# Kernel tuning notes

Measured on AMD Instinct MI355X. Metric: run time of the kernel, lower is better.

Reference implementation:

```python
import jax, jax.numpy as jnp
import numpy as np

B, T, D_MODEL, H, W = 2, 3, 32, 256, 256
N_HEADS, N_LEVELS, N_POINTS = 4, 3, 4


def conv2d(x, w, b, padding=1, dilation=1):
    y = jax.lax.conv_general_dilated(
        x, w, window_strides=(1, 1),
        padding=[(padding, padding), (padding, padding)],
        rhs_dilation=(dilation, dilation),
        dimension_numbers=('NCHW', 'OIHW', 'NCHW'))
    return y + b[None, :, None, None]


def lrelu(x):
    return jnp.where(x >= 0, x, 0.1 * x)


def bilinear_sample(img, x, y):
    # img: (N,C,H,W); x,y: (N,H',W') pixel coords; zero padding outside (grid_sample zeros)
    N, C, Hh, Ww = img.shape
    x0 = jnp.floor(x); y0 = jnp.floor(y)
    lx = x - x0; ly = y - y0
    imf = img.reshape(N, C, Hh * Ww)
    out = jnp.zeros((N, C) + x.shape[1:], img.dtype)
    for dy, dx, wgt in ((0, 0, (1 - lx) * (1 - ly)), (0, 1, lx * (1 - ly)),
                        (1, 0, (1 - lx) * ly), (1, 1, lx * ly)):
        xi = x0 + dx; yi = y0 + dy
        valid = (xi >= 0) & (xi < Ww) & (yi >= 0) & (yi < Hh)
        idx = (jnp.clip(yi, 0, Hh - 1) * Ww + jnp.clip(xi, 0, Ww - 1)).astype(jnp.int32)
        g = jnp.take_along_axis(imf, idx.reshape(N, 1, -1), axis=2).reshape((N, C) + x.shape[1:])
        out = out + g * (wgt * valid)[:, None]
    return out


def flow_warp(x, flow):
    # torch flow_warp with align_corners=True == sampling at pixel coords grid+flow
    N, C, Hh, Ww = x.shape
    gy, gx = jnp.meshgrid(jnp.arange(Hh, dtype=x.dtype), jnp.arange(Ww, dtype=x.dtype), indexing='ij')
    return bilinear_sample(x, gx[None] + flow[:, 0], gy[None] + flow[:, 1])


def ms_deform_attn(value, sampling_locations, attention_weights, h, w):
    # value: (N, L*h*w, Hh, d); loc: (N, Lq, Hh, L, P, 2) in [0,1]; weights: (N, Lq, Hh, L, P)
    # Matches MSDA CUDA kernel: sample at loc*(W,H)-0.5, bilinear, zero pad outside.
    N, _, Hh, d = value.shape
    Lq = sampling_locations.shape[1]
    L, P = sampling_locations.shape[3], sampling_locations.shape[4]
    out = jnp.zeros((N, Lq, Hh, d), value.dtype)
    for l in range(L):
        v = value[:, l * h * w:(l + 1) * h * w].transpose(0, 2, 1, 3)  # (N,Hh,hw,d)
        loc = sampling_locations[:, :, :, l]  # (N,Lq,Hh,P,2)
        x = loc[..., 0] * w - 0.5
        y = loc[..., 1] * h - 0.5
        x0 = jnp.floor(x); y0 = jnp.floor(y)
        lx = x - x0; ly = y - y0
        samp = jnp.zeros((N, Lq, Hh, P, d), value.dtype)
        for dy, dx, wgt in ((0, 0, (1 - lx) * (1 - ly)), (0, 1, lx * (1 - ly)),
                            (1, 0, (1 - lx) * ly), (1, 1, lx * ly)):
            xi = x0 + dx; yi = y0 + dy
            valid = (xi >= 0) & (xi < w) & (yi >= 0) & (yi < h)
            idx = (jnp.clip(yi, 0, h - 1) * w + jnp.clip(xi, 0, w - 1)).astype(jnp.int32)
            idx = idx.transpose(0, 2, 1, 3).reshape(N, Hh, Lq * P)
            g = jnp.take_along_axis(v, idx[..., None], axis=2)  # (N,Hh,Lq*P,d)
            g = g.reshape(N, Hh, Lq, P, d).transpose(0, 2, 1, 3, 4)
            samp = samp + g * (wgt * valid)[..., None]
        out = out + (samp * attention_weights[:, :, :, l][..., None]).sum(axis=3)
    return out.reshape(N, Lq, Hh * d)


def setup_inputs() -> dict:
    key = jax.random.key(0)
    ks = jax.random.split(key, 24)
    def rn(k, shape, s=1.0):
        return jax.random.normal(k, shape, dtype=jnp.float32) * s
    c = D_MODEL
    nofp = N_HEADS * N_LEVELS * N_POINTS
    return {
        'frame': rn(ks[0], (B, T, c, H, W)),
        'srcframe': rn(ks[1], (B, T, c, H, W)),
        'flow_forward': rn(ks[2], (B, T - 1, 2, H, W), 2.0),
        'flow_backward': rn(ks[3], (B, T - 1, 2, H, W), 2.0),
        'W_qk': rn(ks[4], (3 * c, 3 * c + 4, 3, 3), 0.05), 'b_qk': rn(ks[5], (3 * c,), 0.05),
        'W_v': rn(ks[6], (3 * c, 3 * c, 3, 3), 0.05), 'b_v': rn(ks[7], (3 * c,), 0.05),
        'W_vp': rn(ks[8], (c, c, 3, 3), 0.05), 'b_vp': rn(ks[9], (c,), 0.05),
        'W_off': rn(ks[10], (nofp * 2, 3 * c, 3, 3), 0.01), 'b_off': rn(ks[11], (nofp * 2,), 0.5),
        'W_aw': rn(ks[12], (nofp, 3 * c, 3, 3), 0.05), 'b_aw': rn(ks[13], (nofp,), 0.05),
        'W_out': rn(ks[14], (c, c, 3, 3), 0.05), 'b_out': rn(ks[15], (c,), 0.05),
        'W_ffd': rn(ks[16], (c, c, 3, 3), 0.05), 'b_ffd': rn(ks[17], (c,), 0.05),
        'W_ff1': rn(ks[18], (c, 2 * c, 3, 3), 0.05), 'b_ff1': rn(ks[19], (c,), 0.05),
        'W_ff2': rn(ks[20], (c, c, 3, 3), 0.05), 'b_ff2': rn(ks[21], (c,), 0.05),
        'W_fu': rn(ks[22], (c, c, 1, 1), 0.05), 'b_fu': rn(ks[23], (c,), 0.05),
    }


def reference(frame, srcframe, flow_forward, flow_backward,
              W_qk, b_qk, W_v, b_v, W_vp, b_vp, W_off, b_off, W_aw, b_aw,
              W_out, b_out, W_ffd, b_ffd, W_ff1, b_ff1, W_ff2, b_ff2, W_fu, b_fu):
    b, t, c, h, w = frame.shape
    Hh, L, P = N_HEADS, N_LEVELS, N_POINTS
    d = c // Hh
    # flow-warped neighbor frames + flows -> query embedding
    warp01 = flow_warp(frame[:, 0], flow_backward[:, 0])
    warp21 = flow_warp(frame[:, 2], flow_forward[:, 1])
    qk_in = jnp.concatenate([warp01, frame[:, 1], warp21,
                             flow_forward[:, 1], flow_backward[:, 0]], axis=1)
    qureys = lrelu(conv2d(qk_in, W_qk, b_qk))                       # (b, 3c, h, w)
    value = conv2d(frame.reshape(b, t * c, h, w), W_v, b_v)         # (b, 3c, h, w)
    # --- MSDeformAttn_Fusion ---
    val = conv2d(value.reshape(b * t, c, h, w), W_vp, b_vp).reshape(b, t, c, h, w)
    off = conv2d(qureys, W_off, b_off)                               # (b, Hh*L*P*2, h, w)
    aw = conv2d(qureys, W_aw, b_aw)                                  # (b, Hh*L*P, h, w)
    value_flat = val.reshape(b, t, c, h * w).transpose(0, 1, 3, 2).reshape(b, t * h * w, Hh, d)
    off = off.reshape(b, -1, h * w).transpose(0, 2, 1).reshape(b, h * w, Hh, L, P, 2)
    aw = aw.reshape(b, -1, h * w).transpose(0, 2, 1).reshape(b, h * w, Hh, L * P)
    aw = jax.nn.softmax(aw, axis=-1).reshape(b, h * w, Hh, L, P)
    # reference points: pixel centers normalized (masks all zero -> valid_ratios == 1)
    gy, gx = jnp.meshgrid((jnp.arange(h, dtype=off.dtype) + 0.5) / h,
                          (jnp.arange(w, dtype=off.dtype) + 0.5) / w, indexing='ij')
    ref = jnp.stack([gx.reshape(-1), gy.reshape(-1)], -1)            # (hw, 2) (x, y)
    normalizer = jnp.array([w, h], dtype=off.dtype)                  # same for all levels
    loc = ref[None, :, None, None, None, :] + off / normalizer
    attn_out = ms_deform_attn(value_flat, loc, aw, h, w)             # (b, hw, c)
    out = attn_out.reshape(b, h, w, c).transpose(0, 3, 1, 2)
    out = conv2d(out, W_out, b_out)                                  # output_proj
    # --- post-attention ---
    out = conv2d(out, W_ffd, b_ffd) + frame[:, 1]
    tseq = jnp.concatenate([out, srcframe[:, 1]], axis=1)            # (b, 2c, h, w)
    ff = conv2d(lrelu(conv2d(tseq, W_ff1, b_ff1, padding=2, dilation=2)), W_ff2, b_ff2)
    out = out + ff
    out = lrelu(conv2d(out, W_fu, b_fu, padding=0))                  # fusion 1x1
    return out
```

## Files before the change

kernel.cpp:

```cpp
#include <hip/hip_runtime.h>
#include <hip/hip_bf16.h>

typedef __hip_bfloat16 bf16;
typedef unsigned short us;
typedef unsigned int u32;
typedef __attribute__((ext_vector_type(8))) short short8;
typedef __attribute__((ext_vector_type(8))) unsigned short ushortx8;
typedef __attribute__((ext_vector_type(4))) float f32x4;
typedef __attribute__((ext_vector_type(16))) float f32x16;

#define HW 65536
#define IMW 256
#define IMH 256

static __device__ __forceinline__ float u2f(us u) {
  return __uint_as_float(((unsigned)u) << 16);
}
static __device__ __forceinline__ us f2bu(float x) {
  bf16 h = __float2bfloat16(x);
  return *reinterpret_cast<us*>(&h);
}
static __device__ __forceinline__ unsigned pk2(float a, float b) {
  return (unsigned)f2bu(a) | ((unsigned)f2bu(b) << 16);
}

static __device__ __forceinline__ void gload_lds16(const void* g, void* l) {
  __builtin_amdgcn_global_load_lds(
      (const __attribute__((address_space(1))) u32*)g,
      (__attribute__((address_space(3))) u32*)l, 16, 0, 0);
}

struct PrepArgs {
  const float* src[9];
  us* dst[9];
  int OC[9], CIN[9], KPAD[9], LAY[9];
};

__global__ __launch_bounds__(256) void prep_weights(PrepArgs a) {
  int j = blockIdx.y;
  int n = blockIdx.x * 256 + threadIdx.x;
  int OC = a.OC[j], CIN = a.CIN[j], KPAD = a.KPAD[j];
  int tot = 9 * OC * KPAD;
  if (n >= tot) return;
  int oc, k;
  if (a.LAY[j] == 0) {
    int G = OC >> 4, NKC = KPAD >> 5;
    int e = n & 7;
    int m = (n >> 3) & 15;
    int q = (n >> 7) & 3;
    int rest = n >> 9;
    int kc = rest % NKC;
    int tg = rest / NKC;
    int g = tg % G;
    int t = tg / G;
    oc = g * 16 + m;
    k = kc * 32 + q * 8 + e;
    float v = (k < CIN) ? a.src[j][(size_t)(oc * CIN + k) * 9 + t] : 0.f;
    a.dst[j][n] = f2bu(v);
  } else {
    int OCT = OC >> 5, KH = KPAD >> 4;
    int e = n & 7;
    int l = (n >> 3) & 63;
    int rest = n >> 9;
    int jt = rest % OCT;
    int u = rest / OCT;
    int kh = u % KH;
    int t = u / KH;
    oc = jt * 32 + (l & 31);
    k = kh * 16 + (l >> 5) * 8 + e;
    float v = (k < CIN) ? a.src[j][(size_t)(oc * CIN + k) * 9 + t] : 0.f;
    a.dst[j][n] = f2bu(v);
  }
}

__global__ __launch_bounds__(256) void frame_to_nhwc(const float* __restrict__ frame,
                                                     unsigned* __restrict__ fn) {
  int pix = blockIdx.x * 256 + threadIdx.x;
  int b = blockIdx.y;
  const float* s = frame + (size_t)b * 96 * HW + pix;
  unsigned u[48];
#pragma unroll
  for (int j = 0; j < 48; ++j)
    u[j] = pk2(s[(size_t)(2 * j) * HW], s[(size_t)(2 * j + 1) * HW]);
  unsigned* d = fn + ((size_t)b * HW + pix) * 48;
#pragma unroll
  for (int j = 0; j < 12; ++j) {
    uint4 w;
    w.x = u[4 * j]; w.y = u[4 * j + 1]; w.z = u[4 * j + 2]; w.w = u[4 * j + 3];
    *(uint4*)&d[4 * j] = w;
  }
}

static __device__ void warp_nhwc(const us* __restrict__ fn, size_t bbase, int coff,
                                 float x, float y, unsigned* uo) {
  float x0f = floorf(x), y0f = floorf(y);
  float lx = x - x0f, ly = y - y0f;
  int x0 = (int)x0f, y0 = (int)y0f;
  float wt[4] = {(1.f - lx) * (1.f - ly), lx * (1.f - ly), (1.f - lx) * ly, lx * ly};
  float acc[32] = {};
#pragma unroll
  for (int k = 0; k < 4; ++k) {
    int xi = x0 + (k & 1), yi = y0 + (k >> 1);
    if ((unsigned)xi < IMW && (unsigned)yi < IMH) {
      const ushortx8* s =
          (const ushortx8*)(fn + (bbase + (size_t)yi * IMW + xi) * 96 + coff);
      float w = wt[k];
#pragma unroll
      for (int cj = 0; cj < 4; ++cj) {
        ushortx8 vv = s[cj];
#pragma unroll
        for (int e = 0; e < 8; ++e)
          acc[cj * 8 + e] = fmaf(w, u2f(vv[e]), acc[cj * 8 + e]);
      }
    }
  }
#pragma unroll
  for (int j = 0; j < 16; ++j) uo[j] = pk2(acc[2 * j], acc[2 * j + 1]);
}

__global__ __launch_bounds__(256) void build_qkin(
    const us* __restrict__ fn, const float* __restrict__ flowf,
    const float* __restrict__ flowb, unsigned* __restrict__ qk) {
  int pix = blockIdx.x * 256 + threadIdx.x;
  int b = blockIdx.y;
  int px = pix & 255, py = pix >> 8;

  float fbx = flowb[((size_t)(b * 2 + 0) * 2 + 0) * HW + pix];
  float fby = flowb[((size_t)(b * 2 + 0) * 2 + 1) * HW + pix];
  float ffx = flowf[((size_t)(b * 2 + 1) * 2 + 0) * HW + pix];
  float ffy = flowf[((size_t)(b * 2 + 1) * 2 + 1) * HW + pix];

  unsigned u[50];
  {
    const unsigned* s = (const unsigned*)(fn + ((size_t)b * HW + pix) * 96);
#pragma unroll
    for (int j = 0; j < 16; ++j) u[16 + j] = s[16 + j];
  }
  u[48] = pk2(ffx, ffy);
  u[49] = pk2(fbx, fby);

  warp_nhwc(fn, (size_t)b * HW, 0, (float)px + fbx, (float)py + fby, &u[0]);
  warp_nhwc(fn, (size_t)b * HW, 64, (float)px + ffx, (float)py + ffy, &u[32]);

  unsigned* qb = qk + ((size_t)b * HW + pix) * 50;
#pragma unroll
  for (int j = 0; j < 25; ++j) {
    uint2 t;
    t.x = u[2 * j];
    t.y = u[2 * j + 1];
    *(uint2*)(qb + 2 * j) = t;
  }
}

template <int CIN, int CST, int KPAD, int OCT, int KHC, bool LRELU>
__global__ __launch_bounds__(256) void conv3x3_m32(
    const us* __restrict__ in, const us* __restrict__ W2,
    const float* __restrict__ bias, us* __restrict__ out, int out_cst,
    int out_coff) {
  constexpr int COLS = 18, ROWS = 10, HALO = COLS * ROWS;
  constexpr int CIPAD = KPAD + 8;
  constexpr int CH = KPAD / 8;
  constexpr int KH = KPAD / 16;
  constexpr int SPT = KH / KHC;
  constexpr int NSTG = 9 * SPT;
  constexpr int CHB = KHC * OCT;
  __shared__ alignas(16) short lds[HALO * CIPAD];
  __shared__ alignas(16) short wlds[2][CHB * 512];

  const int z = blockIdx.z;
  const int px0 = blockIdx.x * 16, py0 = blockIdx.y * 8;
  const int lane = threadIdx.x & 63;
  const int wv = threadIdx.x >> 6;
  const int n = lane & 31;
  const int sr = n >> 4;
  const int colp = n & 15;
  const int kq = lane >> 5;

  f32x16 acc[OCT];
#pragma unroll
  for (int j = 0; j < OCT; ++j) acc[j] = 0.f;

  for (int c = threadIdx.x; c < HALO * CH; c += 256) {
    int p = c / CH, cb = c - p * CH;
    int row = p / COLS, col = p - row * COLS;
    int gy = py0 + row - 1, gx = px0 + col - 1;
    bool ok = ((unsigned)gy < IMH) && ((unsigned)gx < IMW);
    int ci0 = cb * 8;
    const us* gp = in + ((size_t)z * HW + (size_t)gy * IMW + gx) * CST + ci0;
    if (CIN == KPAD) {
      short8 v = (short8)0;
      if (ok) v = *(const short8*)gp;
      *(short8*)&lds[p * CIPAD + ci0] = v;
    } else {
      uint2 h0; h0.x = 0; h0.y = 0;
      uint2 h1; h1.x = 0; h1.y = 0;
      if (ok && ci0 + 4 <= CIN) h0 = *(const uint2*)gp;
      if (ok && ci0 + 8 <= CIN) h1 = *(const uint2*)(gp + 4);
      *(uint2*)&lds[p * CIPAD + ci0] = h0;
      *(uint2*)&lds[p * CIPAD + ci0 + 4] = h1;
    }
  }

#pragma unroll
  for (int r = 0; r < (CHB + 3) / 4; ++r) {
    int blk = r * 4 + wv;
    if (blk < CHB)
      gload_lds16(W2 + (size_t)(blk * 64 + lane) * 8, &wlds[0][blk * 512]);
  }
  __syncthreads();

  const int lanebase = ((wv * 2 + sr) * COLS + colp) * CIPAD + kq * 8;

  int buf = 0;
#pragma unroll 1
  for (int s = 0; s < NSTG; ++s) {
    if (s + 1 < NSTG) {
      const us* wn = W2 + (size_t)(s + 1) * (CHB * 512);
#pragma unroll
      for (int r = 0; r < (CHB + 3) / 4; ++r) {
        int blk = r * 4 + wv;
        if (blk < CHB)
          gload_lds16(wn + (size_t)(blk * 64 + lane) * 8,
                      &wlds[buf ^ 1][blk * 512]);
      }
    }
    const int t = s / SPT;
    const int kh0 = (s - t * SPT) * KHC;
    const int dy = t / 3 - 1, dx = t - (t / 3) * 3 - 1;
    const int sb = lanebase + ((dy + 1) * COLS + (dx + 1)) * CIPAD + kh0 * 16;
#pragma unroll
    for (int khr = 0; khr < KHC; ++khr) {
      short8 bf = *(const short8*)&lds[sb + khr * 16];
#pragma unroll
      for (int j = 0; j < OCT; ++j) {
        short8 af =
            *(const short8*)&wlds[buf][(khr * OCT + j) * 512 + lane * 8];
        acc[j] =
            __builtin_amdgcn_mfma_f32_32x32x16_bf16(af, bf, acc[j], 0, 0, 0);
      }
    }
    __syncthreads();
    buf ^= 1;
  }

  {
    int row = py0 + wv * 2 + sr;
    int pxc = px0 + colp;
    us* ob = out + ((size_t)z * HW + (size_t)row * IMW + pxc) * out_cst + out_coff;
#pragma unroll
    for (int j = 0; j < OCT; ++j) {
#pragma unroll
      for (int hi = 0; hi < 4; ++hi) {
        int oc0 = j * 32 + hi * 8 + kq * 4;
        f32x4 bb = *(const f32x4*)&bias[oc0];
        float v0 = acc[j][4 * hi + 0] + bb[0];
        float v1 = acc[j][4 * hi + 1] + bb[1];
        float v2 = acc[j][4 * hi + 2] + bb[2];
        float v3 = acc[j][4 * hi + 3] + bb[3];
        if (LRELU) {
          v0 = v0 >= 0.f ? v0 : 0.1f * v0;
          v1 = v1 >= 0.f ? v1 : 0.1f * v1;
          v2 = v2 >= 0.f ? v2 : 0.1f * v2;
          v3 = v3 >= 0.f ? v3 : 0.1f * v3;
        }
        uint2 w;
        w.x = pk2(v0, v1);
        w.y = pk2(v2, v3);
        *(uint2*)&ob[oc0] = w;
      }
    }
  }
}

template <int CIN, int CST, int KPAD, int DIL, int G, int ZDIV, int CSUB,
          int RES, int OUTMODE, bool LRELU>
__global__ __launch_bounds__(256) void conv3x3_mfma(
    const us* __restrict__ in, const us* __restrict__ W2,
    const float* __restrict__ bias, void* __restrict__ out, int out_cst,
    int out_coff, float* __restrict__ outB, const float* __restrict__ res,
    int res_cst, int res_coff) {
  constexpr int OC = G * 16;
  constexpr int COLS = 16 + 2 * DIL;
  constexpr int ROWS = 8 + 2 * DIL;
  constexpr int HALO = ROWS * COLS;
  constexpr int CIPAD = KPAD + 8;
  constexpr int CH = KPAD / 8;
  constexpr int NKC = KPAD / 32;
  constexpr int GW0 = (G + 1) / 2;
  constexpr int NU = 9 * NKC;
  __shared__ alignas(16) short lds[HALO * CIPAD];

  const int z = blockIdx.z;
  const int bin = z / ZDIV;
  const int coff = (z % ZDIV) * CSUB;
  const int px0 = blockIdx.x * 16, py0 = blockIdx.y * 8;
  const int lane = threadIdx.x & 63;
  const int wv = threadIdx.x >> 6;
  const int m = lane & 15, q = lane >> 4;
  const int gh = wv & 1, rh = wv >> 1;
  const int goff = gh * GW0;

  f32x4 acc[GW0][4];
#pragma unroll
  for (int g = 0; g < GW0; ++g)
#pragma unroll
    for (int r = 0; r < 4; ++r) acc[g][r] = 0.f;

  for (int c = threadIdx.x; c < HALO * CH; c += 256) {
    int p = c / CH, cb = c - p * CH;
    int row = p / COLS, col = p - row * COLS;
    int gy = py0 + row - DIL, gx = px0 + col - DIL;
    bool ok = ((unsigned)gy < IMH) && ((unsigned)gx < IMW);
    int ci0 = cb * 8;
    const us* gp = in + ((size_t)bin * HW + (size_t)gy * IMW + gx) * CST + coff + ci0;
    if (CIN == KPAD) {
      short8 v = (short8)0;
      if (ok) v = *(const short8*)gp;
      *(short8*)&lds[p * CIPAD + ci0] = v;
    } else {
      uint2 h0; h0.x = 0; h0.y = 0;
      uint2 h1; h1.x = 0; h1.y = 0;
      if (ok && ci0 + 4 <= CIN) h0 = *(const uint2*)gp;
      if (ok && ci0 + 8 <= CIN) h1 = *(const uint2*)(gp + 4);
      *(uint2*)&lds[p * CIPAD + ci0] = h0;
      *(uint2*)&lds[p * CIPAD + ci0 + 4] = h1;
    }
  }
  __syncthreads();

  const us* wl = W2 + (size_t)lane * 8;
  short8 af[2][GW0];
#pragma unroll
  for (int g = 0; g < GW0; ++g)
    if (goff + g < G)
      af[0][g] = *(const short8*)(wl + (size_t)((goff + g) * NKC) * 512);

#pragma unroll
  for (int u = 0; u < NU; ++u) {
    const int t = u / NKC, kc = u - t * NKC;
    if (u + 1 < NU) {
      const int t1 = (u + 1) / NKC, kc1 = (u + 1) - t1 * NKC;
#pragma unroll
      for (int g = 0; g < GW0; ++g)
        if (goff + g < G)
          af[(u + 1) & 1][g] =
              *(const short8*)(wl + (size_t)((t1 * G + goff + g) * NKC + kc1) * 512);
    }
    const int dy = t / 3 - 1, dx = t - (t / 3) * 3 - 1;
    short8 bfr[4];
#pragma unroll
    for (int r = 0; r < 4; ++r) {
      int rr = rh * 4 + r + DIL + dy * DIL;
      int cc = m + DIL + dx * DIL;
      bfr[r] = *(const short8*)&lds[(rr * COLS + cc) * CIPAD + kc * 32 + q * 8];
    }
#pragma unroll
    for (int g = 0; g < GW0; ++g)
      if (goff + g < G)
#pragma unroll
        for (int r = 0; r < 4; ++r)
          acc[g][r] = __builtin_amdgcn_mfma_f32_16x16x32_bf16(af[u & 1][g], bfr[r],
                                                              acc[g][r], 0, 0, 0);
  }

#pragma unroll
  for (int g = 0; g < GW0; ++g) {
    if (goff + g < G) {
      int oc0 = (goff + g) * 16 + q * 4;
      f32x4 bb = *(const f32x4*)&bias[oc0];
#pragma unroll
      for (int r = 0; r < 4; ++r) {
        int py = py0 + rh * 4 + r;
        int px = px0 + m;
        size_t pix = (size_t)py * IMW + px;
        f32x4 v;
#pragma unroll
        for (int e = 0; e < 4; ++e) {
          float x = acc[g][r][e] + bb[e];
          if (LRELU) x = x >= 0.f ? x : 0.1f * x;
          v[e] = x;
        }
        if (RES == 1) {
          f32x4 rv = *(const f32x4*)&res[((size_t)z * HW + pix) * res_cst + oc0];
#pragma unroll
          for (int e = 0; e < 4; ++e) v[e] += rv[e];
        }
        if (RES == 2) {
#pragma unroll
          for (int e = 0; e < 4; ++e)
            v[e] += res[((size_t)z * res_cst + res_coff + oc0 + e) * HW + pix];
        }
        if (OUTMODE == 0 || OUTMODE == 3) {
          uint2 w;
          w.x = pk2(v[0], v[1]);
          w.y = pk2(v[2], v[3]);
          *(uint2*)&((us*)out)[((size_t)z * HW + pix) * out_cst + out_coff + oc0] = w;
        }
        if (OUTMODE == 2)
          *(f32x4*)&((float*)out)[((size_t)z * HW + pix) * out_cst + oc0] = v;
        if (OUTMODE == 3)
          *(f32x4*)&outB[((size_t)z * HW + pix) * 32 + oc0] = v;
      }
    }
  }
}

__global__ __launch_bounds__(256) void deform_attn(
    const us* __restrict__ valp, const us* __restrict__ off,
    const float* __restrict__ aw, us* __restrict__ outp) {
  int tid = threadIdx.x;
  int hh = tid & 3;
  int pix = blockIdx.x * 64 + (tid >> 2);
  int b = blockIdx.y;
  int px = pix & (IMW - 1), py = pix >> 8;
  float refx = ((float)px + 0.5f) * (1.0f / IMW);
  float refy = ((float)py + 0.5f) * (1.0f / IMH);

  ushortx8 o8[3];
  {
    const ushortx8* ob =
        (const ushortx8*)(off + ((size_t)b * HW + pix) * 96 + hh * 24);
#pragma unroll
    for (int j = 0; j < 3; ++j) o8[j] = ob[j];
  }
  f32x4 a4[3];
  {
    const f32x4* ab = (const f32x4*)(aw + ((size_t)b * HW + pix) * 48 + hh * 12);
#pragma unroll
    for (int j = 0; j < 3; ++j) a4[j] = ab[j];
  }

  float wv[12];
  float mx = -1e30f;
#pragma unroll
  for (int lp = 0; lp < 12; ++lp) {
    wv[lp] = a4[lp >> 2][lp & 3];
    mx = fmaxf(mx, wv[lp]);
  }
  float s = 0.f;
#pragma unroll
  for (int lp = 0; lp < 12; ++lp) {
    wv[lp] = __expf(wv[lp] - mx);
    s += wv[lp];
  }
  float inv = 1.f / s;

  float acc[8] = {0.f, 0.f, 0.f, 0.f, 0.f, 0.f, 0.f, 0.f};
#pragma unroll 1
  for (int l = 0; l < 3; ++l) {
    const us* vbase = valp + ((size_t)(b * 3 + l) * HW) * 32 + hh * 8;
#pragma unroll
    for (int p = 0; p < 4; ++p) {
      int ch = l * 8 + p * 2;
      float ox = u2f(o8[ch >> 3][ch & 7]);
      float oy = u2f(o8[(ch + 1) >> 3][(ch + 1) & 7]);
      float x = (refx + ox * (1.0f / IMW)) * (float)IMW - 0.5f;
      float y = (refy + oy * (1.0f / IMH)) * (float)IMH - 0.5f;
      float x0f = floorf(x), y0f = floorf(y);
      float lx = x - x0f, ly = y - y0f;
      int x0 = (int)x0f, y0 = (int)y0f;
      float a = wv[l * 4 + p] * inv;
      float cw[4] = {(1.f - lx) * (1.f - ly) * a, lx * (1.f - ly) * a,
                     (1.f - lx) * ly * a, lx * ly * a};
#pragma unroll
      for (int k = 0; k < 4; ++k) {
        int xi = x0 + (k & 1), yi = y0 + (k >> 1);
        if ((unsigned)xi < IMW && (unsigned)yi < IMH) {
          const ushortx8 u = *(const ushortx8*)(vbase + (size_t)(yi * IMW + xi) * 32);
          float wgt = cw[k];
#pragma unroll
          for (int dd = 0; dd < 8; ++dd) acc[dd] = fmaf(wgt, u2f(u[dd]), acc[dd]);
        }
      }
    }
  }
  ushortx8 sv;
#pragma unroll
  for (int dd = 0; dd < 8; ++dd) sv[dd] = f2bu(acc[dd]);
  *(ushortx8*)(outp + ((size_t)b * HW + pix) * 32 + hh * 8) = sv;
}

__global__ __launch_bounds__(256) void copy_src(const float* __restrict__ src,
                                                unsigned* __restrict__ out1b) {
  int pix = blockIdx.x * 256 + threadIdx.x;
  int b = blockIdx.y;
  const float* s = src + ((size_t)(b * 3 + 1) * 32) * HW + pix;
  unsigned u[16];
#pragma unroll
  for (int j = 0; j < 16; ++j)
    u[j] = pk2(s[(size_t)(2 * j) * HW], s[(size_t)(2 * j + 1) * HW]);
  unsigned* d = out1b + ((size_t)b * HW + pix) * 32 + 16;
#pragma unroll
  for (int j = 0; j < 4; ++j) {
    uint4 w;
    w.x = u[4 * j]; w.y = u[4 * j + 1]; w.z = u[4 * j + 2]; w.w = u[4 * j + 3];
    *(uint4*)&d[4 * j] = w;
  }
}

__global__ __launch_bounds__(256) void conv1x1_fu(
    const float* __restrict__ in, const float* __restrict__ wgt,
    const float* __restrict__ bias, float* __restrict__ out) {
  int pix = blockIdx.x * 256 + threadIdx.x;
  int b = blockIdx.y;
  float vin[32];
  {
    const f32x4* s = (const f32x4*)(in + ((size_t)b * HW + pix) * 32);
#pragma unroll
    for (int j = 0; j < 8; ++j) {
      f32x4 v = s[j];
#pragma unroll
      for (int e = 0; e < 4; ++e) vin[4 * j + e] = v[e];
    }
  }
#pragma unroll 1
  for (int oc = 0; oc < 32; ++oc) {
    float a = bias[oc];
#pragma unroll
    for (int ci = 0; ci < 32; ++ci) a = fmaf(wgt[oc * 32 + ci], vin[ci], a);
    a = a >= 0.f ? a : 0.1f * a;
    out[((size_t)b * 32 + oc) * HW + pix] = a;
  }
}

extern "C" void kernel_launch(void* const* d_in, const int* in_sizes, int n_in,
                              void* d_out, int out_size, void* d_ws, size_t ws_size,
                              hipStream_t stream) {
  (void)in_sizes; (void)n_in; (void)out_size;
  if (ws_size < 25614592ull * 4) return;

  const float* frame = (const float*)d_in[0];
  const float* srcframe = (const float*)d_in[1];
  const float* flowf = (const float*)d_in[2];
  const float* flowb = (const float*)d_in[3];

  float* ws = (float*)d_ws;
  us* wsu = (us*)d_ws;

  static const int w2off[9] = {0,      110592, 193536, 202752, 285696,
                               327168, 336384, 345600, 364032};
  us* fnhwc = (us*)(ws + 186624);
  unsigned* qk_u = (unsigned*)(ws + 6478080);
  us* qk = (us*)qk_u;
  us* Q = (us*)(ws + 13031680);
  us* V = (us*)(ws + 6478080);
  us* Vp = (us*)(ws + 19323136);
  us* offb = (us*)(ws + 186624);
  float* awb = (float*)(ws + 6478080);
  us* attn = (us*)(ws + 13031680);
  us* convout = (us*)(ws + 13031680 + 2097152);
  us* out1b = (us*)(ws + 6478080);
  unsigned* out1b_u = (unsigned*)out1b;
  float* out1f = (float*)(ws + 19323136);
  us* ff1out = (us*)(ws + 186624);
  float* out2 = (float*)(ws + 13031680);

  {
    PrepArgs pa;
    static const int srcidx[9] = {4, 6, 8, 10, 12, 14, 16, 18, 20};
    static const int OCs[9] = {96, 96, 32, 96, 48, 32, 32, 32, 32};
    static const int CINs[9] = {100, 96, 32, 96, 96, 32, 32, 64, 32};
    static const int KPADs[9] = {128, 96, 32, 96, 96, 32, 32, 64, 32};
    static const int LAYs[9] = {1, 1, 0, 1, 0, 0, 0, 0, 0};
    for (int i = 0; i < 9; ++i) {
      pa.src[i] = (const float*)d_in[srcidx[i]];
      pa.dst[i] = wsu + w2off[i];
      pa.OC[i] = OCs[i];
      pa.CIN[i] = CINs[i];
      pa.KPAD[i] = KPADs[i];
      pa.LAY[i] = LAYs[i];
    }
    prep_weights<<<dim3(432, 9), 256, 0, stream>>>(pa);
  }

  frame_to_nhwc<<<dim3(256, 2), 256, 0, stream>>>(frame, (unsigned*)fnhwc);

  build_qkin<<<dim3(256, 2), 256, 0, stream>>>(fnhwc, flowf, flowb, qk_u);

  dim3 cg2(16, 32, 2);

  conv3x3_m32<100, 100, 128, 3, 4, true><<<cg2, 256, 0, stream>>>(
      qk, wsu + w2off[0], (const float*)d_in[5], Q, 96, 0);

  conv3x3_m32<96, 96, 96, 3, 6, false><<<cg2, 256, 0, stream>>>(
      fnhwc, wsu + w2off[1], (const float*)d_in[7], V, 96, 0);

  conv3x3_mfma<32, 96, 32, 1, 2, 3, 32, 0, 0, false><<<dim3(16, 32, 6), 256, 0, stream>>>(
      V, wsu + w2off[2], (const float*)d_in[9], Vp, 32, 0, nullptr, nullptr, 0, 0);

  conv3x3_m32<96, 96, 96, 3, 6, false><<<cg2, 256, 0, stream>>>(
      Q, wsu + w2off[3], (const float*)d_in[11], offb, 96, 0);

  conv3x3_mfma<96, 96, 96, 1, 3, 1, 0, 0, 2, false><<<cg2, 256, 0, stream>>>(
      Q, wsu + w2off[4], (const float*)d_in[13], awb, 48, 0, nullptr, nullptr, 0, 0);

  deform_attn<<<dim3(1024, 2), 256, 0, stream>>>(Vp, offb, awb, attn);

  conv3x3_mfma<32, 32, 32, 1, 2, 1, 0, 0, 0, false><<<cg2, 256, 0, stream>>>(
      attn, wsu + w2off[5], (const float*)d_in[15], convout, 32, 0, nullptr, nullptr, 0, 0);

  conv3x3_mfma<32, 32, 32, 1, 2, 1, 0, 2, 3, false><<<cg2, 256, 0, stream>>>(
      convout, wsu + w2off[6], (const float*)d_in[17], out1b, 64, 0, out1f, frame, 96, 32);

  copy_src<<<dim3(256, 2), 256, 0, stream>>>(srcframe, out1b_u);

  conv3x3_mfma<64, 64, 64, 2, 2, 1, 0, 0, 0, true><<<cg2, 256, 0, stream>>>(
      out1b, wsu + w2off[7], (const float*)d_in[19], ff1out, 32, 0, nullptr, nullptr, 0, 0);

  conv3x3_mfma<32, 32, 32, 1, 2, 1, 0, 1, 2, false><<<cg2, 256, 0, stream>>>(
      ff1out, wsu + w2off[8], (const float*)d_in[21], out2, 32, 0, nullptr, out1f, 32, 0);

  conv1x1_fu<<<dim3(256, 2), 256, 0, stream>>>(out2, (const float*)d_in[22],
                                               (const float*)d_in[23], (float*)d_out);
}
```

Measured before the change: 465.0 us.

## Split deformable-attention sampling points across two lanes per head

```diff
diff --git a/kernel.cpp b/kernel.cpp
--- a/kernel.cpp
+++ b/kernel.cpp
@@ -6,6 +6,7 @@
 typedef unsigned int u32;
 typedef __attribute__((ext_vector_type(8))) short short8;
 typedef __attribute__((ext_vector_type(8))) unsigned short ushortx8;
+typedef __attribute__((ext_vector_type(2))) float f32x2;
 typedef __attribute__((ext_vector_type(4))) float f32x4;
 typedef __attribute__((ext_vector_type(16))) float f32x16;
 
@@ -409,75 +410,94 @@
     const us* __restrict__ valp, const us* __restrict__ off,
     const float* __restrict__ aw, us* __restrict__ outp) {
   int tid = threadIdx.x;
-  int hh = tid & 3;
-  int pix = blockIdx.x * 64 + (tid >> 2);
+  int half = tid & 1;
+  int hh = (tid >> 1) & 3;
+  int pix = blockIdx.x * 32 + (tid >> 3);
   int b = blockIdx.y;
   int px = pix & (IMW - 1), py = pix >> 8;
-  float refx = ((float)px + 0.5f) * (1.0f / IMW);
-  float refy = ((float)py + 0.5f) * (1.0f / IMH);
-
-  ushortx8 o8[3];
+
+  us os[12];
   {
-    const ushortx8* ob =
-        (const ushortx8*)(off + ((size_t)b * HW + pix) * 96 + hh * 24);
-#pragma unroll
-    for (int j = 0; j < 3; ++j) o8[j] = ob[j];
-  }
-  f32x4 a4[3];
+    const uint2* ob = (const uint2*)(off + ((size_t)b * HW + pix) * 96 +
+                                     hh * 24 + half * 12);
+    uint2 a0 = ob[0], a1 = ob[1], a2 = ob[2];
+    *(uint2*)&os[0] = a0;
+    *(uint2*)&os[4] = a1;
+    *(uint2*)&os[8] = a2;
+  }
+  float wv[6];
   {
-    const f32x4* ab = (const f32x4*)(aw + ((size_t)b * HW + pix) * 48 + hh * 12);
-#pragma unroll
-    for (int j = 0; j < 3; ++j) a4[j] = ab[j];
-  }
-
-  float wv[12];
-  float mx = -1e30f;
-#pragma unroll
-  for (int lp = 0; lp < 12; ++lp) {
-    wv[lp] = a4[lp >> 2][lp & 3];
-    mx = fmaxf(mx, wv[lp]);
-  }
-  float s = 0.f;
-#pragma unroll
-  for (int lp = 0; lp < 12; ++lp) {
-    wv[lp] = __expf(wv[lp] - mx);
-    s += wv[lp];
-  }
-  float inv = 1.f / s;
-
-  float acc[8] = {0.f, 0.f, 0.f, 0.f, 0.f, 0.f, 0.f, 0.f};
-#pragma unroll 1
-  for (int l = 0; l < 3; ++l) {
+    const f32x2* ab = (const f32x2*)(aw + ((size_t)b * HW + pix) * 48 +
+                                     hh * 12 + half * 6);
+    f32x2 a0 = ab[0], a1 = ab[1], a2 = ab[2];
+    wv[0] = a0.x; wv[1] = a0.y; wv[2] = a1.x;
+    wv[3] = a1.y; wv[4] = a2.x; wv[5] = a2.y;
+  }
+
+  float m6 = wv[0];
+#pragma unroll
+  for (int i = 1; i < 6; ++i) m6 = fmaxf(m6, wv[i]);
+  float mx = fmaxf(m6, __shfl_xor(m6, 1));
+  float s6 = 0.f;
+#pragma unroll
+  for (int i = 0; i < 6; ++i) {
+    wv[i] = __expf(wv[i] - mx);
+    s6 += wv[i];
+  }
+  float inv = 1.f / (s6 + __shfl_xor(s6, 1));
+
+  f32x2 acc2[4];
+#pragma unroll
+  for (int j = 0; j < 4; ++j) acc2[j] = 0.f;
+
+#pragma unroll
+  for (int i = 0; i < 6; ++i) {
+    int pp = half * 6 + i;
+    int l = pp >> 2;
     const us* vbase = valp + ((size_t)(b * 3 + l) * HW) * 32 + hh * 8;
-#pragma unroll
-    for (int p = 0; p < 4; ++p) {
-      int ch = l * 8 + p * 2;
-      float ox = u2f(o8[ch >> 3][ch & 7]);
-      float oy = u2f(o8[(ch + 1) >> 3][(ch + 1) & 7]);
-      float x = (refx + ox * (1.0f / IMW)) * (float)IMW - 0.5f;
-      float y = (refy + oy * (1.0f / IMH)) * (float)IMH - 0.5f;
-      float x0f = floorf(x), y0f = floorf(y);
-      float lx = x - x0f, ly = y - y0f;
-      int x0 = (int)x0f, y0 = (int)y0f;
-      float a = wv[l * 4 + p] * inv;
-      float cw[4] = {(1.f - lx) * (1.f - ly) * a, lx * (1.f - ly) * a,
-                     (1.f - lx) * ly * a, lx * ly * a};
-#pragma unroll
-      for (int k = 0; k < 4; ++k) {
-        int xi = x0 + (k & 1), yi = y0 + (k >> 1);
-        if ((unsigned)xi < IMW && (unsigned)yi < IMH) {
-          const ushortx8 u = *(const ushortx8*)(vbase + (size_t)(yi * IMW + xi) * 32);
-          float wgt = cw[k];
-#pragma unroll
-          for (int dd = 0; dd < 8; ++dd) acc[dd] = fmaf(wgt, u2f(u[dd]), acc[dd]);
+    float x = (float)px + u2f(os[2 * i]);
+    float y = (float)py + u2f(os[2 * i + 1]);
+    float x0f = floorf(x), y0f = floorf(y);
+    float lx = x - x0f, ly = y - y0f;
+    int x0 = (int)x0f, y0 = (int)y0f;
+    bool vx0 = (unsigned)x0 < IMW, vx1 = (unsigned)(x0 + 1) < IMW;
+    bool vy0 = (unsigned)y0 < IMH, vy1 = (unsigned)(y0 + 1) < IMH;
+    float a = wv[i] * inv;
+    float ax0 = (1.f - lx) * a, ax1 = lx * a;
+    float w00 = ax0 * (1.f - ly), w01 = ax1 * (1.f - ly);
+    float w10 = ax0 * ly, w11 = ax1 * ly;
+    const us* p00 = vbase + (size_t)((long)(y0 * IMW + x0)) * 32;
+#pragma unroll
+    for (int c = 0; c < 4; ++c) {
+      bool ok = (c & 1 ? vx1 : vx0) && (c & 2 ? vy1 : vy0);
+      float w = (c == 0) ? w00 : (c == 1) ? w01 : (c == 2) ? w10 : w11;
+      const us* p = p00 + (c & 1) * 32 + (c >> 1) * (IMW * 32);
+      if (ok) {
+        uint4 uu = *(const uint4*)p;
+        unsigned uarr[4] = {uu.x, uu.y, uu.z, uu.w};
+#pragma unroll
+        for (int j = 0; j < 4; ++j) {
+          f32x2 v;
+          v.x = __uint_as_float(uarr[j] << 16);
+          v.y = __uint_as_float(uarr[j] & 0xffff0000u);
+          acc2[j] += v * w;
         }
       }
     }
   }
-  ushortx8 sv;
-#pragma unroll
-  for (int dd = 0; dd < 8; ++dd) sv[dd] = f2bu(acc[dd]);
-  *(ushortx8*)(outp + ((size_t)b * HW + pix) * 32 + hh * 8) = sv;
+
+  float accf[8];
+#pragma unroll
+  for (int j = 0; j < 4; ++j) {
+    accf[2 * j] = acc2[j].x + __shfl_xor(acc2[j].x, 1);
+    accf[2 * j + 1] = acc2[j].y + __shfl_xor(acc2[j].y, 1);
+  }
+  if (half == 0) {
+    ushortx8 sv;
+#pragma unroll
+    for (int dd = 0; dd < 8; ++dd) sv[dd] = f2bu(accf[dd]);
+    *(ushortx8*)(outp + ((size_t)b * HW + pix) * 32 + hh * 8) = sv;
+  }
 }
 
 __global__ __launch_bounds__(256) void copy_src(const float* __restrict__ src,
@@ -594,7 +614,7 @@
   conv3x3_mfma<96, 96, 96, 1, 3, 1, 0, 0, 2, false><<<cg2, 256, 0, stream>>>(
       Q, wsu + w2off[4], (const float*)d_in[13], awb, 48, 0, nullptr, nullptr, 0, 0);
 
-  deform_attn<<<dim3(1024, 2), 256, 0, stream>>>(Vp, offb, awb, attn);
+  deform_attn<<<dim3(2048, 2), 256, 0, stream>>>(Vp, offb, awb, attn);
 
   conv3x3_mfma<32, 32, 32, 1, 2, 1, 0, 0, 0, false><<<cg2, 256, 0, stream>>>(
       attn, wsu + w2off[5], (const float*)d_in[15], convout, 32, 0, nullptr, nullptr, 0, 0);
```

After: 461.3 us. About the same (-0.8%).
